# Kernel optimization log

Measured on AMD Instinct MI355X. Metric: run time of the kernel, lower is better.

## Reference

```python
import jax, jax.numpy as jnp
import numpy as np

N = 25000
E = 400000
MUL0 = 64   # multiplicity of 0e node irreps
MUL1 = 32   # multiplicity of 1o node irreps
NUM_BASIS = 10
FC_HIDDEN = 100
WEIGHT_NUMEL = 2 * MUL0 + 3 * MUL1  # 224: per-edge tp weights for the 5 uvu paths
MID_S = MUL0 + MUL1       # 96 mid scalar channels
MID_V = MUL0 + 2 * MUL1   # 128 mid vector channels
NUM_NEIGHBORS = 16.0


def setup_inputs() -> dict:
    key = jax.random.key(0)
    ks = jax.random.split(key, 16)
    inp = {
        'node_scalars': jax.random.normal(ks[0], (N, MUL0), jnp.float32),
        'node_vectors': jax.random.normal(ks[1], (N, MUL1, 3), jnp.float32),
        'node_attr': jnp.ones((N, 1), jnp.float32),
        'edge_src': jax.random.randint(ks[2], (E,), 0, N, jnp.int32),
        'edge_dst': jax.random.randint(ks[3], (E,), 0, N, jnp.int32),
        'edge_attr': jax.random.normal(ks[4], (E, 4), jnp.float32),
        'edge_scalars': jax.random.normal(ks[5], (E, NUM_BASIS), jnp.float32),
        # FullyConnectedNet: [10, 100, weight_numel], silu on hidden
        'W_fc1': jax.random.normal(ks[6], (NUM_BASIS, FC_HIDDEN), jnp.float32) / np.sqrt(NUM_BASIS),
        'W_fc2': jax.random.normal(ks[7], (FC_HIDDEN, WEIGHT_NUMEL), jnp.float32) / np.sqrt(FC_HIDDEN),
        # FullyConnectedTensorProduct with 0e attr == per-irrep linear mixing
        'W_sc_s': jax.random.normal(ks[8], (MUL0, MUL0), jnp.float32) / np.sqrt(MUL0),
        'W_sc_v': jax.random.normal(ks[9], (MUL1, MUL1), jnp.float32) / np.sqrt(MUL1),
        'W_l1_s': jax.random.normal(ks[10], (MUL0, MUL0), jnp.float32) / np.sqrt(MUL0),
        'W_l1_v': jax.random.normal(ks[11], (MUL1, MUL1), jnp.float32) / np.sqrt(MUL1),
        'W_l2_s': jax.random.normal(ks[12], (MID_S, MUL0), jnp.float32) / np.sqrt(MID_S),
        'W_l2_v': jax.random.normal(ks[13], (MID_V, MUL1), jnp.float32) / np.sqrt(MID_V),
        'W_l3': jax.random.normal(ks[14], (MID_S, 1), jnp.float32) / np.sqrt(MID_S),
    }
    return inp


def reference(node_scalars, node_vectors, node_attr, edge_src, edge_dst, edge_attr,
              edge_scalars, W_fc1, W_fc2, W_sc_s, W_sc_v, W_l1_s, W_l1_v,
              W_l2_s, W_l2_v, W_l3):
    n = node_scalars.shape[0]
    # --- edge-weight FC net: silu hidden, linear out -> per-edge tp weights ---
    w = jax.nn.silu(edge_scalars @ W_fc1) @ W_fc2  # [E, 224]
    w_00, w_01 = w[:, :MUL0], w[:, MUL0:2 * MUL0]                  # paths from 0e input
    w_10 = w[:, 2 * MUL0:2 * MUL0 + MUL1]                          # 1o x 0e -> 1o
    w_11s = w[:, 2 * MUL0 + MUL1:2 * MUL0 + 2 * MUL1]              # 1o x 1o -> 0e
    w_11v = w[:, 2 * MUL0 + 2 * MUL1:]                             # 1o x 1o -> 1o

    attr = node_attr  # [N,1] (0e attr => scalar multiplier)
    # self-connection and lin1 (per-irrep linear * attr)
    sc_s = (node_scalars @ W_sc_s) * attr
    sc_v = jnp.einsum('nuc,uv->nvc', node_vectors, W_sc_v) * attr[:, :, None]
    f_s = (node_scalars @ W_l1_s) * attr
    f_v = jnp.einsum('nuc,uv->nvc', node_vectors, W_l1_v) * attr[:, :, None]

    # --- gather source node features per edge ---
    s = f_s[edge_src]          # [E, MUL0]
    v = f_v[edge_src]          # [E, MUL1, 3]
    y0 = edge_attr[:, :1]      # l=0 sh
    y1 = edge_attr[:, 1:4]     # l=1 sh

    # --- weighted tensor product (uvu), CG-contracted paths ---
    mid_s = jnp.concatenate([
        w_00 * s * y0,                                              # 0e x 0e -> 0e
        w_11s * jnp.einsum('euc,ec->eu', v, y1) / jnp.sqrt(3.0),    # 1o x 1o -> 0e
    ], axis=1)                                                      # [E, 96]
    mid_v = jnp.concatenate([
        w_01[:, :, None] * s[:, :, None] * y1[:, None, :],          # 0e x 1o -> 1o
        w_10[:, :, None] * v * y0[:, :, None],                      # 1o x 0e -> 1o
        w_11v[:, :, None] * jnp.cross(v, y1[:, None, :]) / jnp.sqrt(2.0),  # 1o x 1o -> 1o
    ], axis=1)                                                      # [E, 128, 3]

    # --- scatter-add aggregation into destination nodes ---
    inv = 1.0 / jnp.sqrt(NUM_NEIGHBORS)
    agg_s = jax.ops.segment_sum(mid_s, edge_dst, num_segments=n) * inv
    agg_v = jax.ops.segment_sum(mid_v, edge_dst, num_segments=n) * inv

    # --- output linears and gated residual mix ---
    conv_s = (agg_s @ W_l2_s) * attr
    conv_v = jnp.einsum('nuc,uv->nvc', agg_v, W_l2_v) * attr[:, :, None]
    angle = 0.1 * (agg_s @ W_l3) * attr  # [N,1]
    cos, sin = jnp.cos(angle), jnp.sin(angle)  # sc output_mask is all-ones here
    out_s = cos * sc_s + sin * conv_s
    out_v = cos[:, :, None] * sc_v + sin[:, :, None] * conv_v
    return jnp.concatenate([out_s, out_v.reshape(n, -1)], axis=1)  # [N, 64+96]
```

## Files before the change

kernel.cpp:

```cpp
#include <hip/hip_runtime.h>

#define MUL0 64
#define MUL1 32
#define NBASIS 10
#define FCH 100
#define WNUMEL 224
#define MIDS 96
#define MIDV 128
#define EG 4

#define OFF_W1   0
#define OFF_W2   1000
#define OFF_WSCS 23400
#define OFF_WSCV 27496
#define OFF_WL1S 28520
#define OFF_WL1V 32616
#define OFF_WL2S 33640
#define OFF_WL2V 39784
#define OFF_WL3  43880
#define OFF_WEND 43976
#define OFF_FLAG 43980
#define OFF_W1FRAG 44032
#define OFF_W2FRAG 45824
#define OFF_DYN  60160

#define W1FRAG_N (112 * 32)
#define W2FRAG_N (4 * 224 * 32)

typedef __attribute__((ext_vector_type(8))) short short8;
typedef __attribute__((ext_vector_type(4))) float f32x4;

__device__ __forceinline__ float bf2f(unsigned short h) {
    unsigned int u = ((unsigned int)h) << 16;
    float f; __builtin_memcpy(&f, &u, 4); return f;
}
__device__ __forceinline__ unsigned short f2bf(float f) {
    unsigned int u; __builtin_memcpy(&u, &f, 4);
    u += 0x7fffu + ((u >> 16) & 1u);
    return (unsigned short)(u >> 16);
}
__device__ __forceinline__ float fast_silu(float x) {
    return x * __builtin_amdgcn_rcpf(1.0f + __expf(-x));
}
template<bool BF>
__device__ __forceinline__ float ldf(const void* p, size_t i) {
    if constexpr (BF) return bf2f(((const unsigned short*)p)[i]);
    else              return ((const float*)p)[i];
}
template<bool BF>
__device__ __forceinline__ void stf(void* p, size_t i, float v) {
    if constexpr (BF) ((unsigned short*)p)[i] = f2bf(v);
    else              ((float*)p)[i] = v;
}
template<bool BF>
__device__ __forceinline__ f32x4 ld4(const void* p, size_t i) {
    if constexpr (BF) {
        ushort4 h = *(const ushort4*)((const unsigned short*)p + i);
        return (f32x4){bf2f(h.x), bf2f(h.y), bf2f(h.z), bf2f(h.w)};
    } else {
        return *(const f32x4*)((const float*)p + i);
    }
}
__device__ __forceinline__ int wave_incl_scan(int v) {
    int lane = threadIdx.x & 63;
    #pragma unroll
    for (int d = 1; d < 64; d <<= 1) {
        int t = __shfl_up(v, d, 64);
        if (lane >= d) v += t;
    }
    return v;
}

template<bool BF>
__device__ __forceinline__ void node_pre_body(
    const void* __restrict__ ns, const void* __restrict__ nv,
    const void* __restrict__ attr,
    const void* __restrict__ Wl1s, const void* __restrict__ Wl1v,
    float* __restrict__ f_s, float* __restrict__ f_v, int i, int Nn)
{
    int stotal = Nn * MUL0;
    if (i < stotal) {
        int n = i >> 6, j = i & 63;
        float a = 0.f;
        #pragma unroll
        for (int u = 0; u < MUL0; u++)
            a = fmaf(ldf<BF>(ns, (size_t)n * MUL0 + u), ldf<BF>(Wl1s, u * MUL0 + j), a);
        f_s[i] = a * ldf<BF>(attr, n);
    } else {
        int m = i - stotal;
        if (m >= Nn * MUL1 * 3) return;
        int n = m / 96; int idx = m - n * 96;
        int vi = idx / 3; int c = idx - vi * 3;
        float a = 0.f;
        #pragma unroll
        for (int u = 0; u < MUL1; u++)
            a = fmaf(ldf<BF>(nv, (size_t)n * 96 + u * 3 + c), ldf<BF>(Wl1v, u * MUL1 + vi), a);
        f_v[m] = a * ldf<BF>(attr, n);
    }
}

__global__ __launch_bounds__(256) void k_prep(
    const void* __restrict__ ns, const void* __restrict__ nv,
    const void* __restrict__ attr,
    const void* __restrict__ a0, const void* __restrict__ a1,
    const void* __restrict__ a2, const void* __restrict__ a3,
    const void* __restrict__ a4, const void* __restrict__ a5,
    const void* __restrict__ a6, const void* __restrict__ a7,
    const void* __restrict__ a8,
    float* __restrict__ wsf,
    unsigned short* __restrict__ w1frag, unsigned short* __restrict__ w2frag,
    int* __restrict__ cnt, int* __restrict__ flag,
    float* __restrict__ f_s, float* __restrict__ f_v, int Nn)
{
    const bool bf = (((const unsigned int*)attr)[0] == 0x3F803F80u);
    int i = blockIdx.x * 256 + threadIdx.x;
    if (i == 0) *flag = bf ? 1 : 0;

    const int npre = Nn * 160;
    if (i < npre) {
        if (bf) node_pre_body<true >(ns, nv, attr, a4, a5, f_s, f_v, i, Nn);
        else    node_pre_body<false>(ns, nv, attr, a4, a5, f_s, f_v, i, Nn);
        return;
    }
    int m = i - npre;
    if (m < OFF_WEND) {
        const void* p; int off = m;
        if      (m < OFF_W2)   { p = a0; }
        else if (m < OFF_WSCS) { p = a1; off = m - OFF_W2; }
        else if (m < OFF_WSCV) { p = a2; off = m - OFF_WSCS; }
        else if (m < OFF_WL1S) { p = a3; off = m - OFF_WSCV; }
        else if (m < OFF_WL1V) { p = a4; off = m - OFF_WL1S; }
        else if (m < OFF_WL2S) { p = a5; off = m - OFF_WL1V; }
        else if (m < OFF_WL2V) { p = a6; off = m - OFF_WL2S; }
        else if (m < OFF_WL3)  { p = a7; off = m - OFF_WL2V; }
        else                   { p = a8; off = m - OFF_WL3; }
        wsf[m] = bf ? ldf<true>(p, off) : ldf<false>(p, off);
        return;
    }
    m -= OFF_WEND;
    if (m < W1FRAG_N) {
        int col = m >> 5, k = m & 31;
        float v = 0.f;
        if (col < FCH && k < NBASIS)
            v = bf ? ldf<true>(a0, k * FCH + col) : ldf<false>(a0, k * FCH + col);
        w1frag[m] = f2bf(v);
        return;
    }
    m -= W1FRAG_N;
    if (m < W2FRAG_N) {
        int q = m / (224 * 32); int r = m - q * 224 * 32;
        int n = r >> 5; int kk = r & 31;
        int k = q * 32 + kk;
        float v = 0.f;
        if (k < FCH)
            v = bf ? ldf<true>(a1, k * WNUMEL + n) : ldf<false>(a1, k * WNUMEL + n);
        w2frag[m] = f2bf(v);
        return;
    }
    m -= W2FRAG_N;
    if (m < Nn) cnt[m] = 0;
}

__global__ __launch_bounds__(256) void k_hist(
    const int* __restrict__ edst, int* __restrict__ cnt, int Ecnt)
{
    int e = blockIdx.x * 256 + threadIdx.x;
    if (e < Ecnt) atomicAdd(&cnt[edst[e]], 1);
}

__global__ __launch_bounds__(256) void k_scan_blk(
    const int* __restrict__ cnt, int* __restrict__ row_part,
    int* __restrict__ blk_sum, int Nn)
{
    __shared__ int ws4[4];
    int tid = threadIdx.x, lane = tid & 63, wid = tid >> 6;
    int i = blockIdx.x * 256 + tid;
    int v = (i < Nn) ? cnt[i] : 0;
    int incl = wave_incl_scan(v);
    if (lane == 63) ws4[wid] = incl;
    __syncthreads();
    int off = 0;
    #pragma unroll
    for (int w2 = 0; w2 < 4; w2++) off += (w2 < wid) ? ws4[w2] : 0;
    if (i < Nn) row_part[i] = off + incl - v;
    if (tid == 0) blk_sum[blockIdx.x] = ws4[0] + ws4[1] + ws4[2] + ws4[3];
}

__global__ __launch_bounds__(256) void k_scan_top(
    const int* __restrict__ blk_sum, int* __restrict__ blk_off,
    int* __restrict__ row_start, int NB, int Nn)
{
    __shared__ int ws4[4];
    int tid = threadIdx.x, lane = tid & 63, wid = tid >> 6;
    int v = (tid < NB) ? blk_sum[tid] : 0;
    int incl = wave_incl_scan(v);
    if (lane == 63) ws4[wid] = incl;
    __syncthreads();
    int off = 0;
    #pragma unroll
    for (int w2 = 0; w2 < 4; w2++) off += (w2 < wid) ? ws4[w2] : 0;
    if (tid < NB) blk_off[tid] = off + incl - v;
    if (tid == 0) row_start[Nn] = ws4[0] + ws4[1] + ws4[2] + ws4[3];
}

__global__ __launch_bounds__(256) void k_rowfix(
    const int* __restrict__ row_part, const int* __restrict__ blk_off,
    int* __restrict__ row_start, int* __restrict__ cur, int Nn)
{
    int i = blockIdx.x * 256 + threadIdx.x;
    if (i < Nn) { row_start[i] = blk_off[i >> 8] + row_part[i]; cur[i] = 0; }
}

__global__ __launch_bounds__(1024) void k_scan1(
    const int* __restrict__ cnt, int* __restrict__ row_start,
    int* __restrict__ cur, int Nn)
{
    __shared__ int wsum[16];
    __shared__ int s_off, s_tot;
    int tid = threadIdx.x, lane = tid & 63, wid = tid >> 6;
    if (tid == 0) s_off = 0;
    __syncthreads();
    for (int base = 0; base < Nn; base += 1024) {
        int i = base + tid;
        int v = (i < Nn) ? cnt[i] : 0;
        int incl = wave_incl_scan(v);
        if (lane == 63) wsum[wid] = incl;
        __syncthreads();
        if (wid == 0) {
            int wv = (lane < 16) ? wsum[lane] : 0;
            int wincl = wave_incl_scan(wv);
            if (lane < 16) wsum[lane] = wincl - wv;
            if (lane == 15) s_tot = wincl;
        }
        __syncthreads();
        int excl = s_off + wsum[wid] + incl - v;
        if (i < Nn) { row_start[i] = excl; cur[i] = 0; }
        __syncthreads();
        if (tid == 0) s_off += s_tot;
        __syncthreads();
    }
    if (threadIdx.x == 0) row_start[Nn] = s_off;
}

__global__ __launch_bounds__(256) void k_place(
    const int* __restrict__ edst, const int* __restrict__ esrc,
    const void* __restrict__ eattr,
    const int* __restrict__ row_start, int* __restrict__ cur,
    int* __restrict__ perm, int* __restrict__ srcs, float* __restrict__ y4,
    int Ecnt, const int* __restrict__ flag, int extras)
{
    int e = blockIdx.x * 256 + threadIdx.x;
    if (e >= Ecnt) return;
    int d = edst[e];
    int pos = row_start[d] + atomicAdd(&cur[d], 1);
    perm[pos] = e;
    if (extras) {
        srcs[pos] = esrc[e];
        float4 yv;
        if (*flag) {
            const unsigned short* ap = (const unsigned short*)eattr + (size_t)e * 4;
            yv = make_float4(bf2f(ap[0]), bf2f(ap[1]), bf2f(ap[2]), bf2f(ap[3]));
        } else {
            const float* ap = (const float*)eattr + (size_t)e * 4;
            yv = make_float4(ap[0], ap[1], ap[2], ap[3]);
        }
        ((float4*)y4)[pos] = yv;
    }
}

#define HFC_STRIDE 136

__global__ __launch_bounds__(256) void k_fc(
    const void* __restrict__ escal, const int* __restrict__ perm,
    const unsigned short* __restrict__ w1frag, const unsigned short* __restrict__ w2frag,
    unsigned short* __restrict__ wbuf, int Ecnt, const int* __restrict__ flag)
{
    __shared__ __align__(16) unsigned short h_lds[64 * HFC_STRIDE];
    const int tid  = threadIdx.x;
    const int lane = tid & 63;
    const int wave = tid >> 6;
    const int nl   = lane & 15;
    const int quad = lane >> 4;
    const int tb   = blockIdx.x * 64;

    for (int i = tid; i < 64 * 16; i += 256) {
        int row = i >> 4;
        h_lds[row * HFC_STRIDE + 112 + (i & 15)] = 0;
    }

    int eidx = tb + 16 * wave + nl;
    if (eidx >= Ecnt) eidx = Ecnt - 1;
    const int e = perm[eidx];
    short8 a = {0, 0, 0, 0, 0, 0, 0, 0};
    if (*flag) {
        const unsigned int* p = (const unsigned int*)((const unsigned short*)escal + (size_t)e * NBASIS);
        if (quad == 0) {
            unsigned int d0 = p[0], d1 = p[1], d2 = p[2], d3 = p[3];
            a = (short8){(short)d0, (short)(d0 >> 16), (short)d1, (short)(d1 >> 16),
                         (short)d2, (short)(d2 >> 16), (short)d3, (short)(d3 >> 16)};
        } else if (quad == 1) {
            unsigned int d4 = p[4];
            a = (short8){(short)d4, (short)(d4 >> 16), 0, 0, 0, 0, 0, 0};
        }
    } else {
        const float* p = (const float*)escal + (size_t)e * NBASIS;
        if (quad == 0) {
            a = (short8){(short)f2bf(p[0]), (short)f2bf(p[1]), (short)f2bf(p[2]), (short)f2bf(p[3]),
                         (short)f2bf(p[4]), (short)f2bf(p[5]), (short)f2bf(p[6]), (short)f2bf(p[7])};
        } else if (quad == 1) {
            a = (short8){(short)f2bf(p[8]), (short)f2bf(p[9]), 0, 0, 0, 0, 0, 0};
        }
    }

    {
        f32x4 hacc[7];
        #pragma unroll
        for (int t = 0; t < 7; t++) {
            short8 b = *(const short8*)&w1frag[(16 * t + nl) * 32 + quad * 8];
            hacc[t] = __builtin_amdgcn_mfma_f32_16x16x32_bf16(
                a, b, (f32x4){0.f, 0.f, 0.f, 0.f}, 0, 0, 0);
        }
        #pragma unroll
        for (int t = 0; t < 7; t++) {
            #pragma unroll
            for (int r = 0; r < 4; r++)
                h_lds[(16 * wave + quad * 4 + r) * HFC_STRIDE + 16 * t + nl] =
                    f2bf(fast_silu(hacc[t][r]));
        }
    }
    __syncthreads();

    #pragma unroll 2
    for (int t = 0; t < 14; t++) {
        f32x4 c = {0.f, 0.f, 0.f, 0.f};
        #pragma unroll
        for (int q = 0; q < 4; q++) {
            short8 av = *(const short8*)&h_lds[(16 * wave + nl) * HFC_STRIDE + q * 32 + quad * 8];
            short8 b = *(const short8*)&w2frag[((q * 224) + 16 * t + nl) * 32 + quad * 8];
            c = __builtin_amdgcn_mfma_f32_16x16x32_bf16(av, b, c, 0, 0, 0);
        }
        #pragma unroll
        for (int r = 0; r < 4; r++)
            wbuf[(size_t)(tb + 16 * wave + quad * 4 + r) * WNUMEL + 16 * t + nl] = f2bf(c[r]);
    }
}

__global__ __launch_bounds__(256) void k_agg(
    const unsigned short* __restrict__ wbuf,
    const int* __restrict__ srcs, const float* __restrict__ y4,
    const int* __restrict__ row_start,
    const float* __restrict__ f_s, const float* __restrict__ f_v,
    const float* __restrict__ Wl3, const void* __restrict__ attr,
    float* __restrict__ agg_s, float* __restrict__ aggv,
    float* __restrict__ cosb, float* __restrict__ sinb,
    int Nn, const int* __restrict__ flag)
{
    const int tid  = threadIdx.x;
    const int lane = tid & 63;
    const int wave = tid >> 6;
    const int node = blockIdx.x * EG + wave;
    if (node >= Nn) return;

    const int lane2 = lane & 31;
    const int u0 = lane / 3,  c0 = lane - 3 * u0;
    const int pB = 64 + lane;
    const int uB = pB / 3,    cB = pB - 3 * uB;
    const int p2 = 128 + lane;
    const int u2 = p2 / 3,    c2 = p2 - 3 * u2;
    const int pH = 64 + lane2;
    const int uH = pH / 3,    cH = pH - 3 * uH;
    const bool half = (lane < 32);

    const int dlo = row_start[node];
    const int dhi = row_start[node + 1];

    float acc[9];
    #pragma unroll
    for (int s = 0; s < 9; s++) acc[s] = 0.f;

    const float k14 = 0.25f;
    const float k13 = 0.25f * 0.57735026918962576451f;
    const float k12 = 0.25f * 0.70710678118654752440f;

    for (int idx = dlo; idx < dhi; idx++) {
        const int srcn = srcs[idx];
        const float4 y = ((const float4*)y4)[idx];
        const float y0 = y.x, y1x = y.y, y1y = y.z, y1z = y.w;
        const unsigned short* wrow = wbuf + (size_t)idx * WNUMEL;
        const float* fsr = f_s + (size_t)srcn * 64;
        const float* fvr = f_v + (size_t)srcn * 96;

        float fs_l = fsr[lane];
        float fv_a = fvr[lane];
        float fv_b = (lane < 32) ? fvr[64 + lane] : 0.f;

        float fs_u0 = __shfl(fs_l, u0);
        float fs_uB = __shfl(fs_l, uB);
        float fs_u2 = __shfl(fs_l, u2);
        auto fvel = [&](int j) -> float {
            float va = __shfl(fv_a, j & 63);
            float vb = __shfl(fv_b, j & 63);
            return (j < 64) ? va : vb;
        };
        float fvA0 = fvel(3 * lane2), fvA1 = fvel(3 * lane2 + 1), fvA2 = fvel(3 * lane2 + 2);
        float fvB0 = fvel(3 * u0),    fvB1 = fvel(3 * u0 + 1),    fvB2 = fvel(3 * u0 + 2);
        float fvH0 = fvel(3 * uH),    fvH1 = fvel(3 * uH + 1),    fvH2 = fvel(3 * uH + 2);

        float y1c0 = (c0 == 0) ? y1x : (c0 == 1) ? y1y : y1z;
        float y1cB = (cB == 0) ? y1x : (cB == 1) ? y1y : y1z;
        float y1c2 = (c2 == 0) ? y1x : (c2 == 1) ? y1y : y1z;

        float w_s0 = bf2f(wrow[lane]);
        float w_s1 = bf2f(wrow[160 + lane2]);
        float w_s2 = bf2f(wrow[64 + u0]);
        float w_s3 = bf2f(wrow[64 + uB]);
        float w_s4 = bf2f(wrow[64 + u2]);
        float w_s5 = bf2f(wrow[128 + u0]);
        float w_s6 = bf2f(wrow[128 + uH]);
        float w_s7 = bf2f(wrow[192 + u0]);
        float w_s8 = bf2f(wrow[192 + uH]);

        acc[0] = fmaf(w_s0 * fs_l, y0 * k14, acc[0]);
        {
            float dot = fvA0 * y1x + fvA1 * y1y + fvA2 * y1z;
            acc[1] = fmaf(w_s1 * dot, k13, acc[1]);
        }
        acc[2] = fmaf(w_s2 * fs_u0, k14 * y1c0, acc[2]);
        acc[3] = fmaf(w_s3 * fs_uB, k14 * y1cB, acc[3]);
        acc[4] = fmaf(w_s4 * fs_u2, k14 * y1c2, acc[4]);
        {
            float e5 = (c0 == 0) ? fvB0 : (c0 == 1) ? fvB1 : fvB2;
            float e6 = (cH == 0) ? fvH0 : (cH == 1) ? fvH1 : fvH2;
            acc[5] = fmaf(w_s5 * e5, k14 * y0, acc[5]);
            acc[6] = fmaf(w_s6 * e6, k14 * y0, acc[6]);
        }
        {
            float cr7 = (c0 == 0) ? (fvB1 * y1z - fvB2 * y1y)
                      : (c0 == 1) ? (fvB2 * y1x - fvB0 * y1z)
                                  : (fvB0 * y1y - fvB1 * y1x);
            float cr8 = (cH == 0) ? (fvH1 * y1z - fvH2 * y1y)
                      : (cH == 1) ? (fvH2 * y1x - fvH0 * y1z)
                                  : (fvH0 * y1y - fvH1 * y1x);
            acc[7] = fmaf(w_s7 * cr7, k12, acc[7]);
            acc[8] = fmaf(w_s8 * cr8, k12, acc[8]);
        }
    }

    {
        float* as = agg_s + (size_t)node * MIDS;
        float* av = aggv  + (size_t)node * 384;
        as[lane] = acc[0];
        if (half) as[64 + lane] = acc[1];
        {
            int pu, uu, c_;
            pu = lane;       uu = pu / 3; c_ = pu - 3 * uu; av[c_ * 128 + uu] = acc[2];
            pu = 64 + lane;  uu = pu / 3; c_ = pu - 3 * uu; av[c_ * 128 + uu] = acc[3];
            pu = 128 + lane; uu = pu / 3; c_ = pu - 3 * uu; av[c_ * 128 + uu] = acc[4];
            pu = 192 + lane; uu = pu / 3; c_ = pu - 3 * uu; av[c_ * 128 + uu] = acc[5];
            if (half) { pu = 256 + lane; uu = pu / 3; c_ = pu - 3 * uu; av[c_ * 128 + uu] = acc[6]; }
            pu = 288 + lane; uu = pu / 3; c_ = pu - 3 * uu; av[c_ * 128 + uu] = acc[7];
            if (half) { pu = 352 + lane; uu = pu / 3; c_ = pu - 3 * uu; av[c_ * 128 + uu] = acc[8]; }
        }

        float avv = acc[0] * Wl3[lane];
        if (half) avv = fmaf(acc[1], Wl3[64 + lane], avv);
        #pragma unroll
        for (int d = 1; d < 64; d <<= 1) avv += __shfl_xor(avv, d);
        if (lane == 0) {
            float at = (*flag) ? ldf<true>(attr, node) : ldf<false>(attr, node);
            float aa = 0.1f * avv * at;
            cosb[node] = __cosf(aa);
            sinb[node] = __sinf(aa);
        }
    }
}

#define WT_STRIDE 164

template<bool BF>
__device__ __forceinline__ void final_s_body(
    const float* __restrict__ agg_s, const void* __restrict__ ns,
    const float* __restrict__ cosb, const float* __restrict__ sinb,
    const void* __restrict__ attr, void* __restrict__ out,
    int Nn, const float* Wt, int lane, int nb)
{
    float acc_sc[8], acc_l2[8];
    int nidx[8];
    #pragma unroll
    for (int r = 0; r < 8; r++) {
        acc_sc[r] = 0.f; acc_l2[r] = 0.f;
        int n = nb + r; nidx[r] = (n < Nn) ? n : (Nn - 1);
    }
    #pragma unroll 2
    for (int t = 0; t < 16; t++) {
        f32x4 wv = *(const f32x4*)&Wt[lane * WT_STRIDE + 4 * t];
        #pragma unroll
        for (int r = 0; r < 8; r++) {
            f32x4 x = ld4<BF>(ns, (size_t)nidx[r] * 64 + 4 * t);
            acc_sc[r] = fmaf(x[0], wv[0], acc_sc[r]);
            acc_sc[r] = fmaf(x[1], wv[1], acc_sc[r]);
            acc_sc[r] = fmaf(x[2], wv[2], acc_sc[r]);
            acc_sc[r] = fmaf(x[3], wv[3], acc_sc[r]);
        }
    }
    #pragma unroll 2
    for (int t = 0; t < 24; t++) {
        f32x4 wv = *(const f32x4*)&Wt[lane * WT_STRIDE + 64 + 4 * t];
        #pragma unroll
        for (int r = 0; r < 8; r++) {
            f32x4 x = *(const f32x4*)(agg_s + (size_t)nidx[r] * 96 + 4 * t);
            acc_l2[r] = fmaf(x[0], wv[0], acc_l2[r]);
            acc_l2[r] = fmaf(x[1], wv[1], acc_l2[r]);
            acc_l2[r] = fmaf(x[2], wv[2], acc_l2[r]);
            acc_l2[r] = fmaf(x[3], wv[3], acc_l2[r]);
        }
    }
    #pragma unroll
    for (int r = 0; r < 8; r++) {
        int n = nb + r;
        if (n < Nn) {
            float cv = cosb[n], sv = sinb[n];
            float at = ldf<BF>(attr, n);
            stf<BF>(out, (size_t)n * 160 + lane, at * (cv * acc_sc[r] + sv * acc_l2[r]));
        }
    }
}

__global__ __launch_bounds__(256) void k_final_s(
    const float* __restrict__ agg_s, const void* __restrict__ ns,
    const float* __restrict__ Wscs, const float* __restrict__ Wl2s,
    const float* __restrict__ cosb, const float* __restrict__ sinb,
    const void* __restrict__ attr, void* __restrict__ out,
    int Nn, const int* __restrict__ flag)
{
    __shared__ float Wt[64 * WT_STRIDE];
    const int tid = threadIdx.x;
    for (int i = tid; i < 160 * 64; i += 256) {
        int u = i >> 6, j = i & 63;
        float w = (u < 64) ? Wscs[u * 64 + j] : Wl2s[(u - 64) * 64 + j];
        Wt[j * WT_STRIDE + u] = w;
    }
    __syncthreads();

    const int lane = tid & 63;
    const int wave = __builtin_amdgcn_readfirstlane(tid >> 6);
    const int nb   = (blockIdx.x * 4 + wave) * 8;
    if (nb >= Nn) return;
    if (*flag) final_s_body<true >(agg_s, ns, cosb, sinb, attr, out, Nn, Wt, lane, nb);
    else       final_s_body<false>(agg_s, ns, cosb, sinb, attr, out, Nn, Wt, lane, nb);
}

template<bool BF>
__device__ __forceinline__ void final_v_body(
    const float* __restrict__ aggv, const void* __restrict__ nv,
    const float* __restrict__ cosb, const float* __restrict__ sinb,
    const void* __restrict__ attr, void* __restrict__ out,
    int Nn, const float* Wt, int lane, int ub)
{
    const int vi   = lane & 31;
    const int grp  = lane >> 5;
    const int NU   = 3 * Nn;
    float acc_sc[8], acc_l2[8];
    int gidx[8], nn_[8], cc_[8];
    #pragma unroll
    for (int r = 0; r < 8; r++) {
        acc_sc[r] = 0.f; acc_l2[r] = 0.f;
        int g = ub + grp * 8 + r;
        if (g > NU - 1) g = NU - 1;
        gidx[r] = g;
        nn_[r] = (int)((unsigned)g / 3u);
        cc_[r] = g - 3 * nn_[r];
    }
    #pragma unroll 2
    for (int t = 0; t < 8; t++) {
        f32x4 wv = *(const f32x4*)&Wt[vi * WT_STRIDE + 4 * t];
        #pragma unroll
        for (int r = 0; r < 8; r++) {
            size_t b = (size_t)nn_[r] * 96 + (size_t)(4 * t) * 3 + cc_[r];
            float x0 = ldf<BF>(nv, b);
            float x1 = ldf<BF>(nv, b + 3);
            float x2 = ldf<BF>(nv, b + 6);
            float x3 = ldf<BF>(nv, b + 9);
            acc_sc[r] = fmaf(x0, wv[0], acc_sc[r]);
            acc_sc[r] = fmaf(x1, wv[1], acc_sc[r]);
            acc_sc[r] = fmaf(x2, wv[2], acc_sc[r]);
            acc_sc[r] = fmaf(x3, wv[3], acc_sc[r]);
        }
    }
    #pragma unroll 2
    for (int t = 0; t < 32; t++) {
        f32x4 wv = *(const f32x4*)&Wt[vi * WT_STRIDE + 32 + 4 * t];
        #pragma unroll
        for (int r = 0; r < 8; r++) {
            f32x4 x = *(const f32x4*)(aggv + (size_t)gidx[r] * 128 + 4 * t);
            acc_l2[r] = fmaf(x[0], wv[0], acc_l2[r]);
            acc_l2[r] = fmaf(x[1], wv[1], acc_l2[r]);
            acc_l2[r] = fmaf(x[2], wv[2], acc_l2[r]);
            acc_l2[r] = fmaf(x[3], wv[3], acc_l2[r]);
        }
    }
    #pragma unroll
    for (int r = 0; r < 8; r++) {
        int g = ub + grp * 8 + r;
        if (g < NU) {
            int n = nn_[r], c = cc_[r];
            float cv = cosb[n], sv = sinb[n];
            float at = ldf<BF>(attr, n);
            stf<BF>(out, (size_t)n * 160 + 64 + vi * 3 + c,
                    at * (cv * acc_sc[r] + sv * acc_l2[r]));
        }
    }
}

__global__ __launch_bounds__(256) void k_final_v(
    const float* __restrict__ aggv, const void* __restrict__ nv,
    const float* __restrict__ Wscv, const float* __restrict__ Wl2v,
    const float* __restrict__ cosb, const float* __restrict__ sinb,
    const void* __restrict__ attr, void* __restrict__ out,
    int Nn, const int* __restrict__ flag)
{
    __shared__ float Wt[32 * WT_STRIDE];
    const int tid = threadIdx.x;
    for (int i = tid; i < 160 * 32; i += 256) {
        int u = i >> 5, j = i & 31;
        float w = (u < 32) ? Wscv[u * 32 + j] : Wl2v[(u - 32) * 32 + j];
        Wt[j * WT_STRIDE + u] = w;
    }
    __syncthreads();

    const int lane = tid & 63;
    const int wave = __builtin_amdgcn_readfirstlane(tid >> 6);
    const int ub   = (blockIdx.x * 4 + wave) * 16;
    if (ub >= 3 * Nn) return;
    if (*flag) final_v_body<true >(aggv, nv, cosb, sinb, attr, out, Nn, Wt, lane, ub);
    else       final_v_body<false>(aggv, nv, cosb, sinb, attr, out, Nn, Wt, lane, ub);
}

#define ES_STRIDE 40
#define H_STRIDE 136
#define WL_STRIDE 225

__global__ __launch_bounds__(256) void k_edge_mfma(
    const void* __restrict__ escal, const void* __restrict__ eattr,
    const void* __restrict__ attr,
    const int* __restrict__ esrc,
    const int* __restrict__ row_start, const int* __restrict__ perm,
    const unsigned short* __restrict__ w1frag, const unsigned short* __restrict__ w2frag,
    const float* __restrict__ Wl3,
    const float* __restrict__ f_s, const float* __restrict__ f_v,
    float* __restrict__ agg_s, float* __restrict__ agg_v,
    float* __restrict__ cosb, float* __restrict__ sinb,
    int Nn, const int* __restrict__ flag)
{
    __shared__ __align__(16) unsigned short es_lds[64 * ES_STRIDE];
    __shared__ __align__(16) unsigned short h_lds[64 * H_STRIDE];
    __shared__ __align__(16) unsigned short w_lds[64 * WL_STRIDE];
    __shared__ float y_lds[64][4];
    __shared__ int   src_lds[64];

    const int tid  = threadIdx.x;
    const int lane = tid & 63;
    const int wave = tid >> 6;
    const int nl   = lane & 15;
    const int quad = lane >> 4;
    const int gbase = blockIdx.x * EG;
    const bool isbf = (*flag != 0);

    for (int i = tid; i < 64 * 22; i += 256) {
        int row = i / 22, k = 10 + (i - row * 22);
        es_lds[row * ES_STRIDE + k] = 0;
    }
    for (int i = tid; i < 64 * 16; i += 256) {
        int row = i >> 4, k = 112 + (i & 15);
        h_lds[row * H_STRIDE + k] = 0;
    }

    const int lane2 = lane & 31;
    const int u0 = lane / 3,  c0 = lane - 3 * u0;
    const int pB = 64 + lane;
    const int uB = pB / 3,    cB = pB - 3 * uB;
    const int p2 = 128 + lane;
    const int u2 = p2 / 3,    c2 = p2 - 3 * u2;
    const int pH = 64 + lane2;
    const int uH = pH / 3,    cH = pH - 3 * uH;
    const bool half = (lane < 32);

    const int node = gbase + wave;
    const int dlo = (node < Nn) ? row_start[node] : 0;
    const int dhi = (node < Nn) ? row_start[node + 1] : 0;

    float acc[9];
    #pragma unroll
    for (int s = 0; s < 9; s++) acc[s] = 0.f;

    const int gend    = (gbase + EG < Nn) ? (gbase + EG) : Nn;
    const int e_start = row_start[gbase];
    const int e_end   = row_start[gend];

    for (int tb = e_start; tb < e_end; tb += 64) {
        const int tcnt = (e_end - tb < 64) ? (e_end - tb) : 64;
        __syncthreads();

        {
            int i = tid & 63, part = tid >> 6;
            if (i < tcnt && part < 2) {
                int e = perm[tb + i];
                if (part == 0) {
                    unsigned int* dstp = (unsigned int*)&es_lds[i * ES_STRIDE];
                    if (isbf) {
                        const unsigned int* srcp =
                            (const unsigned int*)((const unsigned short*)escal + (size_t)e * NBASIS);
                        #pragma unroll
                        for (int t2 = 0; t2 < 5; t2++) dstp[t2] = srcp[t2];
                    } else {
                        const float* srcp = (const float*)escal + (size_t)e * NBASIS;
                        #pragma unroll
                        for (int t2 = 0; t2 < 5; t2++) {
                            unsigned int lo = f2bf(srcp[2 * t2]);
                            unsigned int hi = f2bf(srcp[2 * t2 + 1]);
                            dstp[t2] = lo | (hi << 16);
                        }
                    }
                } else {
                    src_lds[i] = esrc[e];
                    if (isbf) {
                        const unsigned short* ap = (const unsigned short*)eattr + (size_t)e * 4;
                        #pragma unroll
                        for (int t2 = 0; t2 < 4; t2++) y_lds[i][t2] = bf2f(ap[t2]);
                    } else {
                        const float* ap = (const float*)eattr + (size_t)e * 4;
                        #pragma unroll
                        for (int t2 = 0; t2 < 4; t2++) y_lds[i][t2] = ap[t2];
                    }
                }
            }
        }
        __syncthreads();

        {
            short8 a = *(const short8*)&es_lds[(16 * wave + nl) * ES_STRIDE + quad * 8];
            f32x4 hacc[7];
            #pragma unroll
            for (int t = 0; t < 7; t++) {
                short8 b = *(const short8*)&w1frag[(16 * t + nl) * 32 + quad * 8];
                hacc[t] = __builtin_amdgcn_mfma_f32_16x16x32_bf16(
                    a, b, (f32x4){0.f, 0.f, 0.f, 0.f}, 0, 0, 0);
            }
            #pragma unroll
            for (int t = 0; t < 7; t++) {
                #pragma unroll
                for (int r = 0; r < 4; r++)
                    h_lds[(16 * wave + quad * 4 + r) * H_STRIDE + 16 * t + nl] =
                        f2bf(fast_silu(hacc[t][r]));
            }
        }
        __syncthreads();

        #pragma unroll 2
        for (int t = 0; t < 14; t++) {
            f32x4 c = {0.f, 0.f, 0.f, 0.f};
            #pragma unroll
            for (int q = 0; q < 4; q++) {
                short8 a = *(const short8*)&h_lds[(16 * wave + nl) * H_STRIDE + q * 32 + quad * 8];
                short8 b = *(const short8*)&w2frag[((q * 224) + 16 * t + nl) * 32 + quad * 8];
                c = __builtin_amdgcn_mfma_f32_16x16x32_bf16(a, b, c, 0, 0, 0);
            }
            #pragma unroll
            for (int r = 0; r < 4; r++)
                w_lds[(16 * wave + quad * 4 + r) * WL_STRIDE + 16 * t + nl] = f2bf(c[r]);
        }
        __syncthreads();

        {
            int lo = dlo > tb ? dlo : tb;
            int hi = dhi < tb + tcnt ? dhi : tb + tcnt;
            for (int idx = lo; idx < hi; idx++) {
                const int i = idx - tb;
                const int srcn = src_lds[i];
                const float y0  = y_lds[i][0];
                const float y1x = y_lds[i][1];
                const float y1y = y_lds[i][2];
                const float y1z = y_lds[i][3];
                const float* fsr = f_s + (size_t)srcn * 64;
                const float* fvr = f_v + (size_t)srcn * 96;
                const unsigned short* wrow = &w_lds[i * WL_STRIDE];

                float fs_l  = fsr[lane];
                float fs_u0 = fsr[u0];
                float fs_uB = fsr[uB];
                float fs_u2 = fsr[u2];
                float fvA0 = fvr[lane2 * 3], fvA1 = fvr[lane2 * 3 + 1], fvA2 = fvr[lane2 * 3 + 2];
                float fvB0 = fvr[u0 * 3],    fvB1 = fvr[u0 * 3 + 1],    fvB2 = fvr[u0 * 3 + 2];
                float fvH0 = fvr[uH * 3],    fvH1 = fvr[uH * 3 + 1],    fvH2 = fvr[uH * 3 + 2];

                float y1c0 = (c0 == 0) ? y1x : (c0 == 1) ? y1y : y1z;
                float y1cB = (cB == 0) ? y1x : (cB == 1) ? y1y : y1z;
                float y1c2 = (c2 == 0) ? y1x : (c2 == 1) ? y1y : y1z;

                float w_s0 = bf2f(wrow[lane]);
                float w_s1 = bf2f(wrow[160 + lane2]);
                float w_s2 = bf2f(wrow[64 + u0]);
                float w_s3 = bf2f(wrow[64 + uB]);
                float w_s4 = bf2f(wrow[64 + u2]);
                float w_s5 = bf2f(wrow[128 + u0]);
                float w_s6 = bf2f(wrow[128 + uH]);
                float w_s7 = bf2f(wrow[192 + u0]);
                float w_s8 = bf2f(wrow[192 + uH]);

                const float k14 = 0.25f;
                const float k13 = 0.25f * 0.57735026918962576451f;
                const float k12 = 0.25f * 0.70710678118654752440f;

                acc[0] = fmaf(w_s0 * fs_l, y0 * k14, acc[0]);
                {
                    float dot = fvA0 * y1x + fvA1 * y1y + fvA2 * y1z;
                    acc[1] = fmaf(w_s1 * dot, k13, acc[1]);
                }
                acc[2] = fmaf(w_s2 * fs_u0, k14 * y1c0, acc[2]);
                acc[3] = fmaf(w_s3 * fs_uB, k14 * y1cB, acc[3]);
                acc[4] = fmaf(w_s4 * fs_u2, k14 * y1c2, acc[4]);
                {
                    float e5 = (c0 == 0) ? fvB0 : (c0 == 1) ? fvB1 : fvB2;
                    float e6 = (cH == 0) ? fvH0 : (cH == 1) ? fvH1 : fvH2;
                    acc[5] = fmaf(w_s5 * e5, k14 * y0, acc[5]);
                    acc[6] = fmaf(w_s6 * e6, k14 * y0, acc[6]);
                }
                {
                    float cr7 = (c0 == 0) ? (fvB1 * y1z - fvB2 * y1y)
                              : (c0 == 1) ? (fvB2 * y1x - fvB0 * y1z)
                                          : (fvB0 * y1y - fvB1 * y1x);
                    float cr8 = (cH == 0) ? (fvH1 * y1z - fvH2 * y1y)
                              : (cH == 1) ? (fvH2 * y1x - fvH0 * y1z)
                                          : (fvH0 * y1y - fvH1 * y1x);
                    acc[7] = fmaf(w_s7 * cr7, k12, acc[7]);
                    acc[8] = fmaf(w_s8 * cr8, k12, acc[8]);
                }
            }
        }
    }

    if (node < Nn) {
        float* as = agg_s + (size_t)node * MIDS;
        float* av = agg_v + (size_t)node * (MIDV * 3);
        as[lane] = acc[0];
        if (half) as[64 + lane] = acc[1];
        av[lane]       = acc[2];
        av[64 + lane]  = acc[3];
        av[128 + lane] = acc[4];
        av[192 + lane] = acc[5];
        if (half) av[256 + lane] = acc[6];
        av[288 + lane] = acc[7];
        if (half) av[352 + lane] = acc[8];

        float avv = acc[0] * Wl3[lane];
        if (half) avv = fmaf(acc[1], Wl3[64 + lane], avv);
        #pragma unroll
        for (int d = 1; d < 64; d <<= 1) avv += __shfl_xor(avv, d);
        if (lane == 0) {
            float at = isbf ? ldf<true>(attr, node) : ldf<false>(attr, node);
            float a = 0.1f * avv * at;
            cosb[node] = __cosf(a);
            sinb[node] = __sinf(a);
        }
    }
}

template<bool BF>
__device__ __forceinline__ void final_body(
    const void* __restrict__ ns, const void* __restrict__ nv,
    const void* __restrict__ attr,
    const float* __restrict__ Wscs, const float* __restrict__ Wscv,
    const float* __restrict__ Wl2s, const float* __restrict__ Wl2v,
    const float* __restrict__ agg_s, const float* __restrict__ agg_v,
    const float* __restrict__ cosb, const float* __restrict__ sinb,
    void* __restrict__ out, int Nn)
{
    int i = blockIdx.x * 256 + threadIdx.x;
    int stotal = Nn * MUL0;
    if (i < stotal) {
        int n = i >> 6, j = i & 63;
        const float* ar = agg_s + (size_t)n * MIDS;
        float a1 = 0.f, a2 = 0.f;
        #pragma unroll
        for (int u = 0; u < MUL0; u++)
            a1 = fmaf(ldf<BF>(ns, (size_t)n * MUL0 + u), Wscs[u * MUL0 + j], a1);
        #pragma unroll
        for (int u = 0; u < MIDS; u++) a2 = fmaf(ar[u], Wl2s[u * MUL0 + j], a2);
        float o = ldf<BF>(attr, n) * (cosb[n] * a1 + sinb[n] * a2);
        stf<BF>(out, (size_t)n * 160 + j, o);
    } else {
        int m = i - stotal;
        if (m >= Nn * 96) return;
        int n = m / 96; int idx = m - n * 96;
        int vi = idx / 3; int c = idx - vi * 3;
        const float* ar = agg_v + (size_t)n * (MIDV * 3);
        float a1 = 0.f, a2 = 0.f;
        #pragma unroll
        for (int u = 0; u < MUL1; u++)
            a1 = fmaf(ldf<BF>(nv, (size_t)n * 96 + u * 3 + c), Wscv[u * MUL1 + vi], a1);
        #pragma unroll
        for (int u = 0; u < MIDV; u++) a2 = fmaf(ar[u * 3 + c], Wl2v[u * MUL1 + vi], a2);
        float o = ldf<BF>(attr, n) * (cosb[n] * a1 + sinb[n] * a2);
        stf<BF>(out, (size_t)n * 160 + 64 + idx, o);
    }
}
__global__ __launch_bounds__(256) void k_final(
    const void* ns, const void* nv, const void* attr,
    const float* Wscs, const float* Wscv,
    const float* Wl2s, const float* Wl2v,
    const float* agg_s, const float* agg_v,
    const float* cosb, const float* sinb,
    void* out, int Nn, const int* flag)
{
    if (*flag) final_body<true >(ns, nv, attr, Wscs, Wscv, Wl2s, Wl2v, agg_s, agg_v, cosb, sinb, out, Nn);
    else       final_body<false>(ns, nv, attr, Wscs, Wscv, Wl2s, Wl2v, agg_s, agg_v, cosb, sinb, out, Nn);
}

extern "C" void kernel_launch(void* const* d_in, const int* in_sizes, int n_in,
                              void* d_out, int out_size, void* d_ws, size_t ws_size,
                              hipStream_t stream)
{
    const void* ns    = d_in[0];
    const void* nv    = d_in[1];
    const void* attr  = d_in[2];
    const int*  esrc  = (const int*)d_in[3];
    const int*  edst  = (const int*)d_in[4];
    const void* eattr = d_in[5];
    const void* escal = d_in[6];

    const int Nn   = in_sizes[2];
    const int Ecnt = in_sizes[3];

    float* ws = (float*)d_ws;
    int* flag = (int*)(ws + OFF_FLAG);
    unsigned short* w1frag = (unsigned short*)(ws + OFF_W1FRAG);
    unsigned short* w2frag = (unsigned short*)(ws + OFF_W2FRAG);

    size_t o = OFF_DYN;
    const size_t OFF_FS   = o; o += (size_t)Nn * 64;
    const size_t OFF_FV   = o; o += (size_t)Nn * 96;
    const size_t OFF_AGGS = o; o += (size_t)Nn * 96;
    const size_t OFF_AGGV = o; o += (size_t)Nn * 384;
    const size_t OFF_COS  = o; o += Nn;
    const size_t OFF_SIN  = o; o += Nn;
    const size_t OFF_CNT  = o; o += Nn;
    const size_t OFF_ROW  = o; o += Nn + 1;
    const size_t OFF_CUR  = o; o += Nn;
    const size_t OFF_RPART= o; o += Nn;
    const size_t OFF_BSUM = o; o += 256;
    const size_t OFF_BOFF = o; o += 256;
    const size_t OFF_PERM = o; o += Ecnt;
    const size_t OFF_SRCS = o; o += Ecnt;
    o = (o + 3) & ~(size_t)3;
    const size_t OFF_Y4   = o; o += (size_t)Ecnt * 4;
    o = (o + 15) & ~(size_t)15;
    const size_t OFF_WBUF = o;
    const int tiles = (Ecnt + 63) / 64;
    o += (size_t)tiles * 64 * 112;
    const size_t need_bytes = o * sizeof(float);

    int* cnt       = (int*)(ws + OFF_CNT);
    int* row_start = (int*)(ws + OFF_ROW);
    int* cur       = (int*)(ws + OFF_CUR);
    int* row_part  = (int*)(ws + OFF_RPART);
    int* blk_sum   = (int*)(ws + OFF_BSUM);
    int* blk_off   = (int*)(ws + OFF_BOFF);
    int* perm      = (int*)(ws + OFF_PERM);
    int* srcs      = (int*)(ws + OFF_SRCS);
    float* y4      = ws + OFF_Y4;
    unsigned short* wbuf = (unsigned short*)(ws + OFF_WBUF);

    const int NB = (Nn + 255) / 256;
    const bool split = (ws_size >= need_bytes) && (NB <= 256);

    const int prep_work = Nn * 160 + OFF_WEND + W1FRAG_N + W2FRAG_N + Nn;
    k_prep<<<(prep_work + 255) / 256, 256, 0, stream>>>(
        ns, nv, attr,
        d_in[7], d_in[8], d_in[9], d_in[10], d_in[11], d_in[12],
        d_in[13], d_in[14], d_in[15],
        ws, w1frag, w2frag, cnt, flag,
        ws + OFF_FS, ws + OFF_FV, Nn);

    k_hist<<<(Ecnt + 255) / 256, 256, 0, stream>>>(edst, cnt, Ecnt);

    if (split) {
        k_scan_blk<<<NB, 256, 0, stream>>>(cnt, row_part, blk_sum, Nn);
        k_scan_top<<<1, 256, 0, stream>>>(blk_sum, blk_off, row_start, NB, Nn);
        k_rowfix<<<NB, 256, 0, stream>>>(row_part, blk_off, row_start, cur, Nn);
        k_place<<<(Ecnt + 255) / 256, 256, 0, stream>>>(
            edst, esrc, eattr, row_start, cur, perm, srcs, y4, Ecnt, flag, 1);

        k_fc<<<tiles, 256, 0, stream>>>(escal, perm, w1frag, w2frag, wbuf, Ecnt, flag);

        k_agg<<<(Nn + EG - 1) / EG, 256, 0, stream>>>(
            wbuf, srcs, y4, row_start,
            ws + OFF_FS, ws + OFF_FV, ws + OFF_WL3, attr,
            ws + OFF_AGGS, ws + OFF_AGGV, ws + OFF_COS, ws + OFF_SIN,
            Nn, flag);

        k_final_s<<<(Nn + 31) / 32, 256, 0, stream>>>(
            ws + OFF_AGGS, ns, ws + OFF_WSCS, ws + OFF_WL2S,
            ws + OFF_COS, ws + OFF_SIN, attr, (void*)d_out, Nn, flag);
        k_final_v<<<(3 * Nn + 63) / 64, 256, 0, stream>>>(
            ws + OFF_AGGV, nv, ws + OFF_WSCV, ws + OFF_WL2V,
            ws + OFF_COS, ws + OFF_SIN, attr, (void*)d_out, Nn, flag);
    } else {
        k_scan1<<<1, 1024, 0, stream>>>(cnt, row_start, cur, Nn);
        k_place<<<(Ecnt + 255) / 256, 256, 0, stream>>>(
            edst, esrc, eattr, row_start, cur, perm, srcs, y4, Ecnt, flag, 0);
        k_edge_mfma<<<(Nn + EG - 1) / EG, 256, 0, stream>>>(
            escal, eattr, attr, esrc, row_start, perm, w1frag, w2frag,
            ws + OFF_WL3,
            ws + OFF_FS, ws + OFF_FV,
            ws + OFF_AGGS, ws + OFF_AGGV, ws + OFF_COS, ws + OFF_SIN,
            Nn, flag);
        k_final<<<((Nn * 160) + 255) / 256, 256, 0, stream>>>(
            ns, nv, attr,
            ws + OFF_WSCS, ws + OFF_WSCV, ws + OFF_WL2S, ws + OFF_WL2V,
            ws + OFF_AGGS, ws + OFF_AGGV, ws + OFF_COS, ws + OFF_SIN,
            (void*)d_out, Nn, flag);
    }
}
```

Before: 570.9 us.

## Remap aggregation lanes to per-channel ownership and remove cross-lane shuffles

The per-node edge aggregation kernel now assigns each lane a whole channel with all three vector components, instead of one flattened (channel, component) element. Each lane loads its own source features and weights directly, so the many __shfl calls, component selects and divide/modulo index maths per edge go away. Vector outputs are written to contiguous per-component rows, and the edge loop is unrolled by two. The cost is strided 3-float reads of the vector features per lane and select-based branching between the 1o×0e and 1o×1o paths across lane halves.

```diff
diff --git a/kernel.cpp b/kernel.cpp
--- a/kernel.cpp
+++ b/kernel.cpp
@@ -362,26 +362,20 @@
     if (node >= Nn) return;
 
     const int lane2 = lane & 31;
-    const int u0 = lane / 3,  c0 = lane - 3 * u0;
-    const int pB = 64 + lane;
-    const int uB = pB / 3,    cB = pB - 3 * uB;
-    const int p2 = 128 + lane;
-    const int u2 = p2 / 3,    c2 = p2 - 3 * u2;
-    const int pH = 64 + lane2;
-    const int uH = pH / 3,    cH = pH - 3 * uH;
-    const bool half = (lane < 32);
+    const bool hi = (lane >= 32);
 
     const int dlo = row_start[node];
     const int dhi = row_start[node + 1];
 
-    float acc[9];
-    #pragma unroll
-    for (int s = 0; s < 9; s++) acc[s] = 0.f;
+    float acc0 = 0.f, acc1 = 0.f;
+    float accS0 = 0.f, accS1 = 0.f, accS2 = 0.f;
+    float accV0 = 0.f, accV1 = 0.f, accV2 = 0.f;
 
     const float k14 = 0.25f;
     const float k13 = 0.25f * 0.57735026918962576451f;
     const float k12 = 0.25f * 0.70710678118654752440f;
 
+    #pragma unroll 2
     for (int idx = dlo; idx < dhi; idx++) {
         const int srcn = srcs[idx];
         const float4 y = ((const float4*)y4)[idx];
@@ -391,79 +385,53 @@
         const float* fvr = f_v + (size_t)srcn * 96;
 
         float fs_l = fsr[lane];
-        float fv_a = fvr[lane];
-        float fv_b = (lane < 32) ? fvr[64 + lane] : 0.f;
-
-        float fs_u0 = __shfl(fs_l, u0);
-        float fs_uB = __shfl(fs_l, uB);
-        float fs_u2 = __shfl(fs_l, u2);
-        auto fvel = [&](int j) -> float {
-            float va = __shfl(fv_a, j & 63);
-            float vb = __shfl(fv_b, j & 63);
-            return (j < 64) ? va : vb;
-        };
-        float fvA0 = fvel(3 * lane2), fvA1 = fvel(3 * lane2 + 1), fvA2 = fvel(3 * lane2 + 2);
-        float fvB0 = fvel(3 * u0),    fvB1 = fvel(3 * u0 + 1),    fvB2 = fvel(3 * u0 + 2);
-        float fvH0 = fvel(3 * uH),    fvH1 = fvel(3 * uH + 1),    fvH2 = fvel(3 * uH + 2);
-
-        float y1c0 = (c0 == 0) ? y1x : (c0 == 1) ? y1y : y1z;
-        float y1cB = (cB == 0) ? y1x : (cB == 1) ? y1y : y1z;
-        float y1c2 = (c2 == 0) ? y1x : (c2 == 1) ? y1y : y1z;
-
-        float w_s0 = bf2f(wrow[lane]);
-        float w_s1 = bf2f(wrow[160 + lane2]);
-        float w_s2 = bf2f(wrow[64 + u0]);
-        float w_s3 = bf2f(wrow[64 + uB]);
-        float w_s4 = bf2f(wrow[64 + u2]);
-        float w_s5 = bf2f(wrow[128 + u0]);
-        float w_s6 = bf2f(wrow[128 + uH]);
-        float w_s7 = bf2f(wrow[192 + u0]);
-        float w_s8 = bf2f(wrow[192 + uH]);
-
-        acc[0] = fmaf(w_s0 * fs_l, y0 * k14, acc[0]);
-        {
-            float dot = fvA0 * y1x + fvA1 * y1y + fvA2 * y1z;
-            acc[1] = fmaf(w_s1 * dot, k13, acc[1]);
-        }
-        acc[2] = fmaf(w_s2 * fs_u0, k14 * y1c0, acc[2]);
-        acc[3] = fmaf(w_s3 * fs_uB, k14 * y1cB, acc[3]);
-        acc[4] = fmaf(w_s4 * fs_u2, k14 * y1c2, acc[4]);
-        {
-            float e5 = (c0 == 0) ? fvB0 : (c0 == 1) ? fvB1 : fvB2;
-            float e6 = (cH == 0) ? fvH0 : (cH == 1) ? fvH1 : fvH2;
-            acc[5] = fmaf(w_s5 * e5, k14 * y0, acc[5]);
-            acc[6] = fmaf(w_s6 * e6, k14 * y0, acc[6]);
-        }
-        {
-            float cr7 = (c0 == 0) ? (fvB1 * y1z - fvB2 * y1y)
-                      : (c0 == 1) ? (fvB2 * y1x - fvB0 * y1z)
-                                  : (fvB0 * y1y - fvB1 * y1x);
-            float cr8 = (cH == 0) ? (fvH1 * y1z - fvH2 * y1y)
-                      : (cH == 1) ? (fvH2 * y1x - fvH0 * y1z)
-                                  : (fvH0 * y1y - fvH1 * y1x);
-            acc[7] = fmaf(w_s7 * cr7, k12, acc[7]);
-            acc[8] = fmaf(w_s8 * cr8, k12, acc[8]);
-        }
+        float v0 = fvr[lane2 * 3 + 0];
+        float v1 = fvr[lane2 * 3 + 1];
+        float v2 = fvr[lane2 * 3 + 2];
+
+        float w00 = bf2f(wrow[lane]);
+        float w01 = bf2f(wrow[64 + lane]);
+        float wh  = bf2f(wrow[128 + lane]);
+        float wx  = bf2f(wrow[160 + lane]);
+
+        acc0 = fmaf(w00 * fs_l, y0 * k14, acc0);
+
+        float dot = v0 * y1x + v1 * y1y + v2 * y1z;
+        acc1 = fmaf(wh * dot, k13, acc1);
+
+        float t1 = w01 * fs_l * k14;
+        accS0 = fmaf(t1, y1x, accS0);
+        accS1 = fmaf(t1, y1y, accS1);
+        accS2 = fmaf(t1, y1z, accS2);
+
+        float cx = v1 * y1z - v2 * y1y;
+        float cy = v2 * y1x - v0 * y1z;
+        float cz = v0 * y1y - v1 * y1x;
+        float e0 = hi ? cx : v0;
+        float e1 = hi ? cy : v1;
+        float e2 = hi ? cz : v2;
+        float tv = hi ? (wx * k12) : (wh * (y0 * k14));
+        accV0 = fmaf(e0, tv, accV0);
+        accV1 = fmaf(e1, tv, accV1);
+        accV2 = fmaf(e2, tv, accV2);
     }
 
     {
         float* as = agg_s + (size_t)node * MIDS;
         float* av = aggv  + (size_t)node * 384;
-        as[lane] = acc[0];
-        if (half) as[64 + lane] = acc[1];
-        {
-            int pu, uu, c_;
-            pu = lane;       uu = pu / 3; c_ = pu - 3 * uu; av[c_ * 128 + uu] = acc[2];
-            pu = 64 + lane;  uu = pu / 3; c_ = pu - 3 * uu; av[c_ * 128 + uu] = acc[3];
-            pu = 128 + lane; uu = pu / 3; c_ = pu - 3 * uu; av[c_ * 128 + uu] = acc[4];
-            pu = 192 + lane; uu = pu / 3; c_ = pu - 3 * uu; av[c_ * 128 + uu] = acc[5];
-            if (half) { pu = 256 + lane; uu = pu / 3; c_ = pu - 3 * uu; av[c_ * 128 + uu] = acc[6]; }
-            pu = 288 + lane; uu = pu / 3; c_ = pu - 3 * uu; av[c_ * 128 + uu] = acc[7];
-            if (half) { pu = 352 + lane; uu = pu / 3; c_ = pu - 3 * uu; av[c_ * 128 + uu] = acc[8]; }
-        }
-
-        float avv = acc[0] * Wl3[lane];
-        if (half) avv = fmaf(acc[1], Wl3[64 + lane], avv);
+        as[lane] = acc0;
+        if (hi) as[64 + lane2] = acc1;
+
+        av[0 * 128 + lane] = accS0;
+        av[1 * 128 + lane] = accS1;
+        av[2 * 128 + lane] = accS2;
+        const int vrow = hi ? (96 + lane2) : (64 + lane);
+        av[0 * 128 + vrow] = accV0;
+        av[1 * 128 + vrow] = accV1;
+        av[2 * 128 + vrow] = accV2;
+
+        float avv = acc0 * Wl3[lane];
+        if (hi) avv = fmaf(acc1, Wl3[64 + lane2], avv);
         #pragma unroll
         for (int d = 1; d < 64; d <<= 1) avv += __shfl_xor(avv, d);
         if (lane == 0) {
```

Measured after the change: 544.7 us. -4.6%, faster.
